# Performance work log

Measured on AMD Instinct MI355X. Metric: run time of the kernel, lower is better.

The kernel has to match this reference:

```python
import jax, jax.numpy as jnp
import numpy as np

B, F0, D = 1024, 32, 32
HID = [128, 128, 128]


def setup_inputs() -> dict:
    key = jax.random.key(0)
    ks = jax.random.split(key, 4)
    inputs = jax.random.normal(ks[0], (B, F0, D), dtype=jnp.float32)
    # glorot-like init for conv filters, flattened to (F0*Fk, H)
    def glorot(k, fan_in, fan_out):
        lim = np.sqrt(6.0 / (fan_in + fan_out)).astype(np.float32)
        return jax.random.uniform(k, (fan_in, fan_out), dtype=jnp.float32, minval=-lim, maxval=lim)
    W0 = glorot(ks[1], F0 * F0, HID[0])
    W1 = glorot(ks[2], F0 * HID[0], HID[1])
    W2 = glorot(ks[3], F0 * HID[1], HID[2])
    b0 = jnp.zeros((HID[0],), dtype=jnp.float32)
    b1 = jnp.zeros((HID[1],), dtype=jnp.float32)
    b2 = jnp.zeros((HID[2],), dtype=jnp.float32)
    return {"inputs": inputs, "W0": W0, "W1": W1, "W2": W2,
            "b0": b0, "b1": b1, "b2": b2,
            "field_size": F0, "embedding_size": D}


def _cin_layer(x0, state, W, b):
    # x0: (B, F0, D), state: (B, Fk, D)
    bsz, f0, d = x0.shape
    fk = state.shape[1]
    # per-embedding-dim outer product; flatten (f0, fk) row-major to match
    # tf reshape of matmul(state_split_0, state_split_k^T)
    z = jnp.einsum('bfd,bgd->bdfg', x0, state).reshape(bsz, d, f0 * fk)
    h = z @ W + b  # (B, D, H); 1x1 conv1d == matmul over f0*fk
    # activation is linear (identity)
    return jnp.transpose(h, (0, 2, 1))  # (B, H, D)


def reference(inputs, W0, W1, W2, b0, b1, b2, field_size, embedding_size):
    x0 = inputs.reshape(-1, field_size, embedding_size)
    state = x0
    outputs = []
    for W, b in ((W0, b0), (W1, b1), (W2, b2)):
        fm = _cin_layer(x0, state, W, b)
        state = fm          # skip=False: state and output are the full map
        outputs.append(fm)
    # concat over field axis, sum over embedding dim -> (B, sum(H))
    return jnp.sum(jnp.concatenate(outputs, axis=1), axis=-1)
```

## Files before the change

### kernel.cpp

```cpp
#include <hip/hip_runtime.h>
#include <hip/hip_bf16.h>


typedef __attribute__((ext_vector_type(8))) short short8;
typedef __attribute__((ext_vector_type(8))) __bf16 bf16x8;
typedef __attribute__((ext_vector_type(16))) float f32x16;
typedef __attribute__((ext_vector_type(4))) unsigned short u16x4;

#define DEVINL static __device__ __forceinline__

DEVINL unsigned short f2bf_rne(float f) {
  unsigned int u = __builtin_bit_cast(unsigned int, f);
  unsigned int r = u + 0x7fffu + ((u >> 16) & 1u);
  return (unsigned short)(r >> 16);
}

template <typename V>
DEVINL auto mfma_32x32x16_bf16(V a, V b, f32x16 c, int)
    -> decltype(__builtin_amdgcn_mfma_f32_32x32x16_bf16(a, b, c, 0, 0, 0)) {
  return __builtin_amdgcn_mfma_f32_32x32x16_bf16(a, b, c, 0, 0, 0);
}
template <typename V>
DEVINL f32x16 mfma_32x32x16_bf16(V a, V b, f32x16 c, long) {
  return __builtin_amdgcn_mfma_f32_32x32x16_bf16(
      __builtin_bit_cast(bf16x8, a), __builtin_bit_cast(bf16x8, b), c, 0, 0, 0);
}
DEVINL f32x16 mfma_bf16(short8 a, short8 b, f32x16 c) {
  return mfma_32x32x16_bf16(a, b, c, 0);
}

__global__ void pack_w_kernel(const float* __restrict__ W0,
                              const float* __restrict__ W1,
                              const float* __restrict__ W2,
                              unsigned short* __restrict__ Wt) {
  __shared__ float tile[8][132];
  const int u = blockIdx.x;
  const float* W; int FK, f, kb, base;
  if (u < 128)      { W = W0; FK = 32;  f = u >> 2;         kb = u & 3;          base = 0; }
  else if (u < 640) { W = W1; FK = 128; f = (u - 128) >> 4; kb = (u - 128) & 15; base = 131072; }
  else              { W = W2; FK = 128; f = (u - 640) >> 4; kb = (u - 640) & 15; base = 655360; }
  const int t = threadIdx.x;
#pragma unroll
  for (int i = 0; i < 4; ++i) {
    const int e = t + i * 256;
    const int kk = e >> 7, h = e & 127;
    tile[kk][h] = W[(f * FK + kb * 8 + kk) * 128 + h];
  }
  __syncthreads();
  unsigned short* dst = Wt + base + f * (FK / 8) * 1024 + kb * 1024;
  const int h = t >> 1;
  const int j0 = (t & 1) * 4;
  u16x4 v;
  v.x = f2bf_rne(tile[j0 + 0][h]);
  v.y = f2bf_rne(tile[j0 + 1][h]);
  v.z = f2bf_rne(tile[j0 + 2][h]);
  v.w = f2bf_rne(tile[j0 + 3][h]);
  *(u16x4*)&dst[t * 4] = v;
}

template <int KQ, int STEPS, int LAYER>
DEVINL void run_layer(const unsigned short* __restrict__ WtL,
                      const float* __restrict__ bias,
                      const float* __restrict__ x0g,
                      float* __restrict__ outp, int outoff,
                      unsigned int* SB,
                      int wgb0, int mrow, int npair, int l31, int half) {
  __syncthreads();

  int4 sfr[2][KQ];
  const int rb = npair * 64;
#pragma unroll
  for (int nt = 0; nt < 2; ++nt) {
    const int r = rb + nt * 32 + l31;
#pragma unroll
    for (int kq = 0; kq < KQ; ++kq) {
      const int row0 = kq * 8 + half * 4;
      int4 v;
      v.x = (int)SB[(row0 + 0) * 128 + r];
      v.y = (int)SB[(row0 + 1) * 128 + r];
      v.z = (int)SB[(row0 + 2) * 128 + r];
      v.w = (int)SB[(row0 + 3) * 128 + r];
      sfr[nt][kq] = v;
    }
  }

  f32x16 zv;
#pragma unroll
  for (int e = 0; e < 16; ++e) zv[e] = 0.f;
  f32x16 outacc[2] = {zv, zv};

  const char* gb = (const char*)WtL +
                   (size_t)(half * 2048 + (mrow * 32 + l31) * 16);
  const int xb0 = (wgb0 + npair * 2 + 0) * 1024 + l31;
  const int xb1 = (wgb0 + npair * 2 + 1) * 1024 + l31;

  auto ldq = [&](short8* wv, int q) {
#pragma unroll
    for (int i = 0; i < 4; ++i)
      wv[i] = *(const short8*)(gb + (size_t)q * 16384 + i * 4096);
  };

  if constexpr (KQ == 8) {
    short8 w0[4], w1[4], w2[4], w3[4];
    float xc00 = x0g[xb0], xc01 = x0g[xb1];
    float xc10 = x0g[xb0 + 32], xc11 = x0g[xb1 + 32];
    ldq(w0, 0);
    ldq(w1, 1);
    __syncthreads();

    auto doFld = [&](const short8* qa, const short8* qb, float xs0, float xs1) {
      f32x16 Y0, Y1;
#pragma unroll
      for (int i = 0; i < 4; ++i) {
        const short8 s0 = __builtin_bit_cast(short8, sfr[0][i]);
        const short8 s1 = __builtin_bit_cast(short8, sfr[1][i]);
        Y0 = mfma_bf16(qa[i], s0, i == 0 ? zv : Y0);
        Y1 = mfma_bf16(qa[i], s1, i == 0 ? zv : Y1);
      }
#pragma unroll
      for (int i = 0; i < 4; ++i) {
        const short8 s0 = __builtin_bit_cast(short8, sfr[0][4 + i]);
        const short8 s1 = __builtin_bit_cast(short8, sfr[1][4 + i]);
        Y0 = mfma_bf16(qb[i], s0, Y0);
        Y1 = mfma_bf16(qb[i], s1, Y1);
      }
#pragma unroll
      for (int e = 0; e < 16; ++e) {
        outacc[0][e] += xs0 * Y0[e];
        outacc[1][e] += xs1 * Y1[e];
      }
    };

#pragma unroll 1
    for (int it = 0; it < 16; ++it) {
      const int f = 2 * it;
      float xn00 = xc00, xn01 = xc01, xn10 = xc10, xn11 = xc11;
      if (it < 15) {
        xn00 = x0g[xb0 + (f + 2) * 32]; xn01 = x0g[xb1 + (f + 2) * 32];
        xn10 = x0g[xb0 + (f + 3) * 32]; xn11 = x0g[xb1 + (f + 3) * 32];
      }
      ldq(w2, 4 * it + 2);
      ldq(w3, 4 * it + 3);
      doFld(w0, w1, xc00, xc01);
      if (it < 15) {
        ldq(w0, 4 * it + 4);
        ldq(w1, 4 * it + 5);
      }
      doFld(w2, w3, xc10, xc11);
      xc00 = xn00; xc01 = xn01; xc10 = xn10; xc11 = xn11;
    }
  } else {
    short8 wa[4], wb[4];
    float xa0 = x0g[xb0], xa1 = x0g[xb1];
    float xa2 = x0g[xb0 + 32], xa3 = x0g[xb1 + 32];
    ldq(wa, 0);
    __syncthreads();

    const short8 s00 = __builtin_bit_cast(short8, sfr[0][0]);
    const short8 s01 = __builtin_bit_cast(short8, sfr[0][1]);
    const short8 s10 = __builtin_bit_cast(short8, sfr[1][0]);
    const short8 s11 = __builtin_bit_cast(short8, sfr[1][1]);
    auto doQ = [&](const short8* wv, float x0a, float x1a, float x0b,
                   float x1b) {
      f32x16 Y0 = mfma_bf16(wv[0], s00, zv);
      Y0 = mfma_bf16(wv[1], s01, Y0);
      f32x16 Y1 = mfma_bf16(wv[0], s10, zv);
      Y1 = mfma_bf16(wv[1], s11, Y1);
#pragma unroll
      for (int e = 0; e < 16; ++e) {
        outacc[0][e] += x0a * Y0[e];
        outacc[1][e] += x1a * Y1[e];
      }
      Y0 = mfma_bf16(wv[2], s00, zv);
      Y0 = mfma_bf16(wv[3], s01, Y0);
      Y1 = mfma_bf16(wv[2], s10, zv);
      Y1 = mfma_bf16(wv[3], s11, Y1);
#pragma unroll
      for (int e = 0; e < 16; ++e) {
        outacc[0][e] += x0b * Y0[e];
        outacc[1][e] += x1b * Y1[e];
      }
    };

#pragma unroll 1
    for (int q2 = 0; q2 < 8; ++q2) {
      const int q = 2 * q2;
      const float xm0 = x0g[xb0 + (2 * q + 2) * 32];
      const float xm1 = x0g[xb1 + (2 * q + 2) * 32];
      const float xm2 = x0g[xb0 + (2 * q + 3) * 32];
      const float xm3 = x0g[xb1 + (2 * q + 3) * 32];
      ldq(wb, q + 1);
      float xn0 = xa0, xn1 = xa1, xn2 = xa2, xn3 = xa3;
      if (q2 < 7) {
        xn0 = x0g[xb0 + (2 * q + 4) * 32];
        xn1 = x0g[xb1 + (2 * q + 4) * 32];
        xn2 = x0g[xb0 + (2 * q + 5) * 32];
        xn3 = x0g[xb1 + (2 * q + 5) * 32];
      }
      doQ(wa, xa0, xa1, xa2, xa3);
      if (q2 < 7) ldq(wa, q + 2);
      doQ(wb, xm0, xm1, xm2, xm3);
      xa0 = xn0; xa1 = xn1; xa2 = xn2; xa3 = xn3;
    }
  }

  float bv[16];
#pragma unroll
  for (int e = 0; e < 16; ++e)
    bv[e] = bias[mrow * 32 + (e & 3) + 8 * (e >> 2) + 4 * half];

  if constexpr (LAYER < 2) {
#pragma unroll
    for (int nt = 0; nt < 2; ++nt) {
      const int r = rb + nt * 32 + l31;
#pragma unroll
      for (int g = 0; g < 4; ++g) {
        const int h2 = mrow * 16 + 4 * g + 2 * half;
        const float v0 = outacc[nt][4 * g + 0] + bv[4 * g + 0];
        const float v1 = outacc[nt][4 * g + 1] + bv[4 * g + 1];
        const float v2 = outacc[nt][4 * g + 2] + bv[4 * g + 2];
        const float v3 = outacc[nt][4 * g + 3] + bv[4 * g + 3];
        SB[h2 * 128 + r] =
            (unsigned)f2bf_rne(v0) | ((unsigned)f2bf_rne(v1) << 16);
        SB[(h2 + 1) * 128 + r] =
            (unsigned)f2bf_rne(v2) | ((unsigned)f2bf_rne(v3) << 16);
      }
    }
  }

#pragma unroll
  for (int nt = 0; nt < 2; ++nt) {
    float sv[16];
#pragma unroll
    for (int e = 0; e < 16; ++e) {
      float v = outacc[nt][e];
      v += __shfl_xor(v, 1);
      v += __shfl_xor(v, 2);
      v += __shfl_xor(v, 4);
      v += __shfl_xor(v, 8);
      v += __shfl_xor(v, 16);
      sv[e] = v + 32.0f * bv[e];
    }
    if (l31 == 0) {
      const int b = npair * 2 + nt;
#pragma unroll
      for (int g = 0; g < 4; ++g) {
        const int h = mrow * 32 + 8 * g + 4 * half;
        float4 o = {sv[4 * g + 0], sv[4 * g + 1], sv[4 * g + 2], sv[4 * g + 3]};
        *(float4*)&outp[b * 384 + outoff + h] = o;
      }
    }
  }
}

__global__ __launch_bounds__(512, 1) void cin_kernel(
    const float* __restrict__ x0g, const unsigned short* __restrict__ Wt,
    const float* __restrict__ b0, const float* __restrict__ b1,
    const float* __restrict__ b2, float* __restrict__ out) {
  __shared__ unsigned int SB[64 * 128];

  const int t = threadIdx.x;
  const int lane = t & 63;
  const int w = t >> 6;
  const int mrow = w & 3;
  const int npair = w >> 2;
  const int l31 = lane & 31, half = lane >> 5;
  const int wgb0 = blockIdx.x * 4;

#pragma unroll
  for (int s = 0; s < 4; ++s) {
    const int i = t + s * 512;
    const int r = i & 127, g2 = i >> 7;
    const float* p = &x0g[(wgb0 + (r >> 5)) * 1024 + (2 * g2) * 32 + (r & 31)];
    SB[g2 * 128 + r] =
        (unsigned)f2bf_rne(p[0]) | ((unsigned)f2bf_rne(p[32]) << 16);
  }

  float* outp = out + (size_t)wgb0 * 384;
  run_layer<2, 8, 0>(Wt, b0, x0g, outp, 0, SB, wgb0, mrow, npair, l31, half);
  run_layer<8, 32, 1>(Wt + 131072, b1, x0g, outp, 128, SB,
                      wgb0, mrow, npair, l31, half);
  run_layer<8, 32, 2>(Wt + 655360, b2, x0g, outp, 256, SB,
                      wgb0, mrow, npair, l31, half);
}

extern "C" void kernel_launch(void* const* d_in, const int* in_sizes, int n_in,
                              void* d_out, int out_size, void* d_ws, size_t ws_size,
                              hipStream_t stream) {
  (void)in_sizes; (void)n_in; (void)out_size; (void)ws_size;
  const float* x0 = (const float*)d_in[0];
  const float* W0 = (const float*)d_in[1];
  const float* W1 = (const float*)d_in[2];
  const float* W2 = (const float*)d_in[3];
  const float* b0 = (const float*)d_in[4];
  const float* b1 = (const float*)d_in[5];
  const float* b2 = (const float*)d_in[6];
  unsigned short* Wt = (unsigned short*)d_ws;

  pack_w_kernel<<<1152, 256, 0, stream>>>(W0, W1, W2, Wt);
  cin_kernel<<<256, 512, 0, stream>>>(x0, Wt, b0, b1, b2, (float*)d_out);
}
```

Before: 154.5 us.

## Specialize last CIN layer by reducing over embedding dim before the weight GEMM

Replaces the generic third-layer path with a specialized routine. It exploits the fact that the final output sums over the embedding dimension, so the outer-product state is contracted over d first via a small MFMA, giving a (batch, f0*fk) vector. That vector then goes through a GEMV-like MFMA pass against the packed weights, with two accumulators and double-buffered weight and LDS loads. This avoids materializing the full per-d z tensor and the full B×D×H GEMM for the last layer, at the cost of an extra bf16 rounding of the reduced intermediate and a split-K reduction through shared memory.

Result: faster. 133.4 us (-13.6%).

```diff
diff --git a/kernel.cpp b/kernel.cpp
--- a/kernel.cpp
+++ b/kernel.cpp
@@ -253,6 +253,131 @@
   }
 }
 
+DEVINL void run_layer2_fast(const unsigned short* __restrict__ WtL,
+                            const float* __restrict__ bias,
+                            const float* __restrict__ x0g,
+                            float* __restrict__ outp,
+                            unsigned int* SB, int wgb0,
+                            int w, int l31, int half, int tid) {
+  __syncthreads();
+
+  f32x16 zv;
+#pragma unroll
+  for (int e = 0; e < 16; ++e) zv[e] = 0.f;
+
+  const int bw = w >> 1, gh = w & 1;
+  short8 a1[2];
+  {
+    const float* xr = &x0g[(size_t)((wgb0 + bw) * 32 + l31) * 32];
+#pragma unroll
+    for (int kq = 0; kq < 2; ++kq) {
+      const int d0 = kq * 16 + half * 8;
+      union { short8 v; unsigned short u[8]; } t;
+#pragma unroll
+      for (int j = 0; j < 8; ++j) t.u[j] = f2bf_rne(xr[d0 + j]);
+      a1[kq] = t.v;
+    }
+  }
+  short8 bfr[2][2];
+#pragma unroll
+  for (int nt = 0; nt < 2; ++nt) {
+    const int g = gh * 64 + nt * 32 + l31;
+    const unsigned int* row = &SB[(g >> 1) * 128 + bw * 32];
+    const int sh = (g & 1) * 16;
+#pragma unroll
+    for (int kq = 0; kq < 2; ++kq) {
+      const int d0 = kq * 16 + half * 8;
+      union { short8 v; unsigned short u[8]; } t;
+#pragma unroll
+      for (int j = 0; j < 8; ++j)
+        t.u[j] = (unsigned short)(row[d0 + j] >> sh);
+      bfr[nt][kq] = t.v;
+    }
+  }
+  f32x16 ua[2];
+#pragma unroll
+  for (int nt = 0; nt < 2; ++nt) {
+    ua[nt] = mfma_bf16(a1[0], bfr[nt][0], zv);
+    ua[nt] = mfma_bf16(a1[1], bfr[nt][1], ua[nt]);
+  }
+  __syncthreads();
+
+  unsigned short* U16 = (unsigned short*)SB;
+#pragma unroll
+  for (int nt = 0; nt < 2; ++nt) {
+    const int g = gh * 64 + nt * 32 + l31;
+#pragma unroll
+    for (int reg = 0; reg < 16; ++reg) {
+      const int f = (reg & 3) + 8 * (reg >> 2) + 4 * half;
+      const int k = f * 128 + g;
+      U16[(k >> 1) * 8 + bw * 2 + (k & 1)] = f2bf_rne(ua[nt][reg]);
+    }
+  }
+  __syncthreads();
+
+  const int mt = w & 3, kh = w >> 2;
+  const char* gb = (const char*)WtL +
+                   (size_t)(half * 2048 + (mt * 32 + l31) * 16);
+  const int bl = l31 & 3;
+
+  auto ldq2 = [&](short8* wv, int q) {
+#pragma unroll
+    for (int i = 0; i < 4; ++i)
+      wv[i] = *(const short8*)(gb + (size_t)q * 16384 + i * 4096);
+  };
+  auto breadq = [&](short8* bv, int q) {
+#pragma unroll
+    for (int i = 0; i < 4; ++i) {
+      const int row0 = (q * 4 + i) * 8 + half * 4;
+      int4 v;
+      v.x = (int)SB[(row0 + 0) * 4 + bl];
+      v.y = (int)SB[(row0 + 1) * 4 + bl];
+      v.z = (int)SB[(row0 + 2) * 4 + bl];
+      v.w = (int)SB[(row0 + 3) * 4 + bl];
+      bv[i] = __builtin_bit_cast(short8, v);
+    }
+  };
+
+  f32x16 acc0 = zv, acc1 = zv;
+  short8 qa[4], qb[4], Ba[4], Bb[4];
+  const int q0 = kh * 32;
+  ldq2(qa, q0);
+  breadq(Ba, q0);
+#pragma unroll 1
+  for (int qq = 0; qq < 16; ++qq) {
+    const int q = q0 + 2 * qq;
+    ldq2(qb, q + 1);
+    breadq(Bb, q + 1);
+#pragma unroll
+    for (int i = 0; i < 4; ++i) acc0 = mfma_bf16(qa[i], Ba[i], acc0);
+    if (qq < 15) {
+      ldq2(qa, q + 2);
+      breadq(Ba, q + 2);
+    }
+#pragma unroll
+    for (int i = 0; i < 4; ++i) acc1 = mfma_bf16(qb[i], Bb[i], acc1);
+  }
+#pragma unroll
+  for (int e = 0; e < 16; ++e) acc0[e] += acc1[e];
+
+  __syncthreads();
+
+  float* P = (float*)SB;
+  if (l31 < 4) {
+#pragma unroll
+    for (int reg = 0; reg < 16; ++reg) {
+      const int h = mt * 32 + (reg & 3) + 8 * (reg >> 2) + 4 * half;
+      P[(l31 * 128 + h) * 2 + kh] = acc0[reg];
+    }
+  }
+  __syncthreads();
+  {
+    const int b = tid >> 7, h = tid & 127;
+    const float v = P[tid * 2] + P[tid * 2 + 1] + 32.0f * bias[h];
+    outp[b * 384 + 256 + h] = v;
+  }
+}
+
 __global__ __launch_bounds__(512, 1) void cin_kernel(
     const float* __restrict__ x0g, const unsigned short* __restrict__ Wt,
     const float* __restrict__ b0, const float* __restrict__ b1,
@@ -280,8 +405,7 @@
   run_layer<2, 8, 0>(Wt, b0, x0g, outp, 0, SB, wgb0, mrow, npair, l31, half);
   run_layer<8, 32, 1>(Wt + 131072, b1, x0g, outp, 128, SB,
                       wgb0, mrow, npair, l31, half);
-  run_layer<8, 32, 2>(Wt + 655360, b2, x0g, outp, 256, SB,
-                      wgb0, mrow, npair, l31, half);
+  run_layer2_fast(Wt + 655360, b2, x0g, outp, SB, wgb0, w, l31, half, t);
 }
 
 extern "C" void kernel_launch(void* const* d_in, const int* in_sizes, int n_in,
```
